# Kernel tuning notes

Hardware: AMD Instinct MI355X
Metric: run time of the kernel (lower is better)

The kernel has to match this reference:

```python
import jax, jax.numpy as jnp
import numpy as np
from jax import lax

T, B, H = 8192, 16, 256
D0, D1, D2 = 64, 64, 128


def setup_inputs() -> dict:
    key = jax.random.key(0)
    ks = jax.random.split(key, 16)
    k = 1.0 / np.sqrt(H)  # torch LSTMCell default init scale

    def u(kk, shape):
        return jax.random.uniform(kk, shape, jnp.float32, -k, k)

    inp = {
        "x0": jax.random.normal(ks[0], (T, B, D0), jnp.float32),
        "x1": jax.random.normal(ks[1], (T // 2, B, D1), jnp.float32),
        "x2": jax.random.normal(ks[2], (T // 4, B, D2), jnp.float32),
    }
    # one LSTMCell per possible concatenated input size: a=256 (all), b=128 (two), c=64 (one)
    sizes = [("a", D0 + D1 + D2), ("b", D0 + D1), ("c", D0)]
    i = 3
    for name, s in sizes:
        inp[f"W_ih_{name}"] = u(ks[i], (4 * H, s)); i += 1
        inp[f"W_hh_{name}"] = u(ks[i], (4 * H, H)); i += 1
        inp[f"b_ih_{name}"] = u(ks[i], (4 * H,)); i += 1
        inp[f"b_hh_{name}"] = u(ks[i], (4 * H,)); i += 1
    return inp


def _cell(x, h, c, Wih, Whh, bih, bhh):
    # torch.nn.LSTMCell: gates = x W_ih^T + b_ih + h W_hh^T + b_hh; order i,f,g,o
    g = x @ Wih.T + bih + h @ Whh.T + bhh
    i, f, gg, o = jnp.split(g, 4, axis=-1)
    c2 = jax.nn.sigmoid(f) * c + jax.nn.sigmoid(i) * jnp.tanh(gg)
    h2 = jax.nn.sigmoid(o) * jnp.tanh(c2)
    return h2, c2


def reference(x0, x1, x2,
              W_ih_a, W_hh_a, b_ih_a, b_hh_a,
              W_ih_b, W_hh_b, b_ih_b, b_hh_b,
              W_ih_c, W_hh_c, b_ih_c, b_hh_c):
    # ratios = [1, 2, 4]; active sets are nested: t%4==0 -> all 3, t%2==0 -> first 2, else first only
    def step(carry, t):
        h, c = carry

        def br_all(_):
            xt = jnp.concatenate([x0[t], x1[t // 2], x2[t // 4]], axis=-1)  # [B, 256]
            return _cell(xt, h, c, W_ih_a, W_hh_a, b_ih_a, b_hh_a)

        def br_two(_):
            xt = jnp.concatenate([x0[t], x1[t // 2]], axis=-1)  # [B, 128]
            return _cell(xt, h, c, W_ih_b, W_hh_b, b_ih_b, b_hh_b)

        def br_one(_):
            return _cell(x0[t], h, c, W_ih_c, W_hh_c, b_ih_c, b_hh_c)  # [B, 64]

        branch = jnp.where(t % 4 == 0, 0, jnp.where(t % 2 == 0, 1, 2))
        h2, c2 = lax.switch(branch, [br_all, br_two, br_one], None)
        return (h2, c2), h2

    h0 = jnp.zeros((B, H), jnp.float32)
    (_, _), ys = lax.scan(step, (h0, h0), jnp.arange(T))
    return ys  # [T, B, H]
```

## Files before the change

kernel.cpp:

```cpp
#include <hip/hip_runtime.h>
#include <stdint.h>


typedef _Float16 half8 __attribute__((ext_vector_type(8)));
typedef float floatx4 __attribute__((ext_vector_type(4)));
typedef unsigned int u32x4 __attribute__((ext_vector_type(4)));

#define T_STEPS 8192
#define NWG 16

__device__ __forceinline__ float fsig(float x) {
    return __builtin_amdgcn_rcpf(1.0f + __expf(-x));
}
__device__ __forceinline__ float ftanh(float x) {
    return 1.0f - 2.0f * __builtin_amdgcn_rcpf(1.0f + __expf(2.0f * x));
}

__device__ __forceinline__ half8 cvt8(floatx4 a, floatx4 b) {
    half8 h;
    h[0] = (_Float16)a[0]; h[1] = (_Float16)a[1]; h[2] = (_Float16)a[2]; h[3] = (_Float16)a[3];
    h[4] = (_Float16)b[0]; h[5] = (_Float16)b[1]; h[6] = (_Float16)b[2]; h[7] = (_Float16)b[3];
    return h;
}
__device__ __forceinline__ half8 ld8w(const float* p) {
    floatx4 a = *(const floatx4*)p;
    floatx4 b = *(const floatx4*)(p + 4);
    return cvt8(a, b);
}

__device__ __forceinline__ void ld64_sc1(const void* p, u32x4& a, u32x4& b, u32x4& c, u32x4& d) {
    asm volatile(
        "global_load_dwordx4 %0, %4, off sc1\n\t"
        "global_load_dwordx4 %1, %4, off offset:16 sc1\n\t"
        "global_load_dwordx4 %2, %4, off offset:32 sc1\n\t"
        "global_load_dwordx4 %3, %4, off offset:48 sc1\n\t"
        "s_waitcnt vmcnt(0)"
        : "=&v"(a), "=&v"(b), "=&v"(c), "=&v"(d)
        : "v"(p)
        : "memory");
}
__device__ __forceinline__ void st16_sc1(void* p, u32x4 v) {
    asm volatile("global_store_dwordx4 %0, %1, off sc1" :: "v"(p), "v"(v) : "memory");
}

__global__ __launch_bounds__(256, 1) void lstm_kernel(
    const float* __restrict__ x0, const float* __restrict__ x1, const float* __restrict__ x2,
    const float* __restrict__ Wih_a, const float* __restrict__ Whh_a,
    const float* __restrict__ bih_a, const float* __restrict__ bhh_a,
    const float* __restrict__ Wih_b, const float* __restrict__ Whh_b,
    const float* __restrict__ bih_b, const float* __restrict__ bhh_b,
    const float* __restrict__ Wih_c, const float* __restrict__ Whh_c,
    const float* __restrict__ bih_c, const float* __restrict__ bhh_c,
    float* __restrict__ out, uint8_t* __restrict__ ws, int smask)
{
    const int tid = threadIdx.x;
    const int g   = blockIdx.x;
    const int w   = tid >> 6;
    const int l   = tid & 63;
    const int n   = l & 15;
    const int mg  = l >> 4;
    const int up  = n & 3;
    const int gt  = n >> 2;
    const int unit = g * 16 + w * 4 + up;
    const int R    = gt * 256 + unit;

    uint8_t* hring = ws;

    __shared__ _Float16 XB[2][16][264];
    __shared__ _Float16 HB[16][264];

    half8 wfa[16], wfb[12], wfc[10];
    {
        const int ko = mg * 8;
        #pragma unroll
        for (int kt = 0; kt < 8; ++kt) wfa[kt]     = ld8w(Wih_a + (size_t)R * 256 + kt * 32 + ko);
        #pragma unroll
        for (int kt = 0; kt < 8; ++kt) wfa[8 + kt] = ld8w(Whh_a + (size_t)R * 256 + kt * 32 + ko);
        #pragma unroll
        for (int kt = 0; kt < 4; ++kt) wfb[kt]     = ld8w(Wih_b + (size_t)R * 128 + kt * 32 + ko);
        #pragma unroll
        for (int kt = 0; kt < 8; ++kt) wfb[4 + kt] = ld8w(Whh_b + (size_t)R * 256 + kt * 32 + ko);
        #pragma unroll
        for (int kt = 0; kt < 2; ++kt) wfc[kt]     = ld8w(Wih_c + (size_t)R * 64  + kt * 32 + ko);
        #pragma unroll
        for (int kt = 0; kt < 8; ++kt) wfc[2 + kt] = ld8w(Whh_c + (size_t)R * 256 + kt * 32 + ko);
    }
    const float ba = bih_a[R] + bhh_a[R];
    const float bb = bih_b[R] + bhh_b[R];
    const float bc = bih_c[R] + bhh_c[R];

    const int pm  = (tid & 127) >> 3;
    const int pcg = (tid & 7) * 8;
    const int qm  = tid >> 4;
    const int qcg = (tid & 15) * 8;

    floatx4 z4 = {0.f, 0.f, 0.f, 0.f};
    floatx4 a0A = z4, a1A = z4, b0A = z4, b1A = z4;
    floatx4 a0B = z4, a1B = z4, b0B = z4, b1B = z4;

    auto issue = [&](int ts, floatx4& A0, floatx4& A1, floatx4& B0, floatx4& B1) {
        const int brn = ((ts & 3) == 0) ? 0 : (((ts & 1) == 0) ? 1 : 2);
        if (tid < 128) {
            const floatx4* s = (const floatx4*)(x0 + (size_t)ts * 1024 + pm * 64 + pcg);
            A0 = s[0]; A1 = s[1];
        } else if (brn < 2) {
            const floatx4* s = (const floatx4*)(x1 + (size_t)(ts >> 1) * 1024 + pm * 64 + pcg);
            A0 = s[0]; A1 = s[1];
        }
        if (brn == 0) {
            const floatx4* s = (const floatx4*)(x2 + (size_t)(ts >> 2) * 2048 + qm * 128 + qcg);
            B0 = s[0]; B1 = s[1];
        }
    };
    auto stage = [&](int ts, floatx4 A0, floatx4 A1, floatx4 B0, floatx4 B1) {
        const int brn = ((ts & 3) == 0) ? 0 : (((ts & 1) == 0) ? 1 : 2);
        const int xb  = ts & 1;
        if (tid < 128)     *(half8*)&XB[xb][pm][pcg]       = cvt8(A0, A1);
        else if (brn < 2)  *(half8*)&XB[xb][pm][64 + pcg]  = cvt8(A0, A1);
        if (brn == 0)      *(half8*)&XB[xb][qm][128 + qcg] = cvt8(B0, B1);
    };

    {
        floatx4 A0 = z4, A1 = z4, B0 = z4, B1 = z4;
        issue(0, A0, A1, B0, B1);
        stage(0, A0, A1, B0, B1);
    }
    issue(1, a0B, a1B, b0B, b1B);

    float cst[4] = {0.f, 0.f, 0.f, 0.f};

    for (int t = 0; t < T_STEPS; ++t) {
        __syncthreads();

        const int br = ((t & 3) == 0) ? 0 : (((t & 1) == 0) ? 1 : 2);
        const int ao = mg * 8;
        const int xb = t & 1;

        floatx4 ac0 = {0.f, 0.f, 0.f, 0.f}, ac1 = {0.f, 0.f, 0.f, 0.f};
        if (br == 0) {
            #pragma unroll
            for (int kt = 0; kt < 8; kt += 2) {
                ac0 = __builtin_amdgcn_mfma_f32_16x16x32_f16(
                    *(const half8*)&XB[xb][n][kt * 32 + ao], wfa[kt], ac0, 0, 0, 0);
                ac1 = __builtin_amdgcn_mfma_f32_16x16x32_f16(
                    *(const half8*)&XB[xb][n][(kt + 1) * 32 + ao], wfa[kt + 1], ac1, 0, 0, 0);
            }
        } else if (br == 1) {
            #pragma unroll
            for (int kt = 0; kt < 4; kt += 2) {
                ac0 = __builtin_amdgcn_mfma_f32_16x16x32_f16(
                    *(const half8*)&XB[xb][n][kt * 32 + ao], wfb[kt], ac0, 0, 0, 0);
                ac1 = __builtin_amdgcn_mfma_f32_16x16x32_f16(
                    *(const half8*)&XB[xb][n][(kt + 1) * 32 + ao], wfb[kt + 1], ac1, 0, 0, 0);
            }
        } else {
            ac0 = __builtin_amdgcn_mfma_f32_16x16x32_f16(
                *(const half8*)&XB[xb][n][ao], wfc[0], ac0, 0, 0, 0);
            ac1 = __builtin_amdgcn_mfma_f32_16x16x32_f16(
                *(const half8*)&XB[xb][n][32 + ao], wfc[1], ac1, 0, 0, 0);
        }

        {
            const int row = tid >> 4, u = tid & 15;
            _Float16* dst = &HB[row][u * 16];
            if (t == 0) {
                *(u32x4*)dst       = (u32x4)0u;
                *(u32x4*)(dst + 8) = (u32x4)0u;
            } else {
                const uint32_t want = (uint32_t)t;
                const uint8_t* src = hring + (size_t)((t - 1) & smask) * 16384
                                   + (size_t)row * 1024 + (size_t)u * 64;
                u32x4 a, b, c, d;
                for (;;) {
                    ld64_sc1(src, a, b, c, d);
                    if (a[1] == want && a[3] == want && b[1] == want && b[3] == want &&
                        c[1] == want && c[3] == want && d[1] == want && d[3] == want)
                        break;
                }
                u32x4 lo = {a[0], a[2], b[0], b[2]};
                u32x4 hi = {c[0], c[2], d[0], d[2]};
                *(u32x4*)dst       = lo;
                *(u32x4*)(dst + 8) = hi;
            }
        }

        if (t + 2 < T_STEPS) {
            if ((t & 1) == 0) issue(t + 2, a0A, a1A, b0A, b1A);
            else              issue(t + 2, a0B, a1B, b0B, b1B);
        }

        __syncthreads();

        if (br == 0) {
            #pragma unroll
            for (int kt = 0; kt < 8; kt += 2) {
                ac0 = __builtin_amdgcn_mfma_f32_16x16x32_f16(
                    *(const half8*)&HB[n][kt * 32 + ao], wfa[8 + kt], ac0, 0, 0, 0);
                ac1 = __builtin_amdgcn_mfma_f32_16x16x32_f16(
                    *(const half8*)&HB[n][(kt + 1) * 32 + ao], wfa[9 + kt], ac1, 0, 0, 0);
            }
        } else if (br == 1) {
            #pragma unroll
            for (int kt = 0; kt < 8; kt += 2) {
                ac0 = __builtin_amdgcn_mfma_f32_16x16x32_f16(
                    *(const half8*)&HB[n][kt * 32 + ao], wfb[4 + kt], ac0, 0, 0, 0);
                ac1 = __builtin_amdgcn_mfma_f32_16x16x32_f16(
                    *(const half8*)&HB[n][(kt + 1) * 32 + ao], wfb[5 + kt], ac1, 0, 0, 0);
            }
        } else {
            #pragma unroll
            for (int kt = 0; kt < 8; kt += 2) {
                ac0 = __builtin_amdgcn_mfma_f32_16x16x32_f16(
                    *(const half8*)&HB[n][kt * 32 + ao], wfc[2 + kt], ac0, 0, 0, 0);
                ac1 = __builtin_amdgcn_mfma_f32_16x16x32_f16(
                    *(const half8*)&HB[n][(kt + 1) * 32 + ao], wfc[3 + kt], ac1, 0, 0, 0);
            }
        }
        const floatx4 acc = ac0 + ac1;

        const float bsel = (br == 0) ? ba : ((br == 1) ? bb : bc);
        float tv[4];
        #pragma unroll
        for (int r = 0; r < 4; ++r) {
            const float gv = acc[r] + bsel;
            tv[r] = (gt == 2) ? ftanh(gv) : fsig(gv);
        }
        float h2v[4];
        const int b0 = l & ~12;
        #pragma unroll
        for (int r = 0; r < 4; ++r) {
            const float vi = __shfl(tv[r], b0,      64);
            const float vf = __shfl(tv[r], b0 + 4,  64);
            const float vg = __shfl(tv[r], b0 + 8,  64);
            const float vo = __shfl(tv[r], b0 + 12, 64);
            const float c2 = vf * cst[r] + vi * vg;
            cst[r] = c2;
            h2v[r] = vo * ftanh(c2);
        }

        {
            uint8_t* sb = hring + (size_t)(t & smask) * 16384 + (size_t)(8 * g + 2 * w) * 8;
            const int s0 = l & ~15;
            #pragma unroll
            for (int r = 0; r < 4; ++r) {
                const unsigned hv =
                    (unsigned)__builtin_bit_cast(unsigned short, (_Float16)h2v[r]);
                const unsigned v0 = (unsigned)__shfl((int)hv, s0,     64);
                const unsigned v1 = (unsigned)__shfl((int)hv, s0 + 1, 64);
                const unsigned v2 = (unsigned)__shfl((int)hv, s0 + 2, 64);
                const unsigned v3 = (unsigned)__shfl((int)hv, s0 + 3, 64);
                if (n == 0) {
                    u32x4 pk = { (v0 & 0xffffu) | (v1 << 16), (unsigned)(t + 1),
                                 (v2 & 0xffffu) | (v3 << 16), (unsigned)(t + 1) };
                    st16_sc1(sb + (size_t)(mg * 4 + r) * 1024, pk);
                }
            }
        }

        if (gt == 0) {
            float* op = out + (size_t)t * 4096 + (size_t)(mg * 4) * 256 + unit;
            #pragma unroll
            for (int r = 0; r < 4; ++r) op[r * 256] = h2v[r];
        }

        if (t + 1 < T_STEPS) {
            if (t & 1) stage(t + 1, a0A, a1A, b0A, b1A);
            else       stage(t + 1, a0B, a1B, b0B, b1B);
        }
    }
}

extern "C" void kernel_launch(void* const* d_in, const int* in_sizes, int n_in,
                              void* d_out, int out_size, void* d_ws, size_t ws_size,
                              hipStream_t stream) {
    (void)in_sizes; (void)n_in; (void)out_size;
    const int smask = (ws_size >= 4 * 16384) ? 3 : 1;
    hipLaunchKernelGGL(lstm_kernel, dim3(NWG), dim3(256), 0, stream,
        (const float*)d_in[0], (const float*)d_in[1], (const float*)d_in[2],
        (const float*)d_in[3], (const float*)d_in[4], (const float*)d_in[5], (const float*)d_in[6],
        (const float*)d_in[7], (const float*)d_in[8], (const float*)d_in[9], (const float*)d_in[10],
        (const float*)d_in[11], (const float*)d_in[12], (const float*)d_in[13], (const float*)d_in[14],
        (float*)d_out, (uint8_t*)d_ws, smask);
}
```

Before: 20.01 ms.

## Gather h publish through LDS into one wave and defer output stores

Each step's new h fragment is now written to a small LDS staging tile and published to the global ring by a single wave with one 16-byte store per lane, instead of shuffles plus scattered stores from every wave. Wave 3 no longer polls the ring. Waves 0-1 poll as before, and wave 2 polls a double-width region so rows 8-15 are still covered. The output store for step t is deferred to the next iteration, so it overlaps the poll instead of sitting on the critical path. Barriers become a raw s_barrier that waits only on LDS counters. The cost is an extra barrier per step and more load imbalance among the polling waves.

```diff
diff --git a/kernel.cpp b/kernel.cpp
--- a/kernel.cpp
+++ b/kernel.cpp
@@ -14,6 +14,12 @@
 }
 __device__ __forceinline__ float ftanh(float x) {
     return 1.0f - 2.0f * __builtin_amdgcn_rcpf(1.0f + __expf(2.0f * x));
+}
+
+__device__ __forceinline__ void bar_lds() {
+    asm volatile("s_waitcnt lgkmcnt(0)" ::: "memory");
+    __builtin_amdgcn_s_barrier();
+    asm volatile("" ::: "memory");
 }
 
 __device__ __forceinline__ half8 cvt8(floatx4 a, floatx4 b) {
@@ -36,6 +42,24 @@
         "global_load_dwordx4 %3, %4, off offset:48 sc1\n\t"
         "s_waitcnt vmcnt(0)"
         : "=&v"(a), "=&v"(b), "=&v"(c), "=&v"(d)
+        : "v"(p)
+        : "memory");
+}
+__device__ __forceinline__ void ld128_sc1(const void* p,
+        u32x4& r0, u32x4& r1, u32x4& r2, u32x4& r3,
+        u32x4& r4, u32x4& r5, u32x4& r6, u32x4& r7) {
+    asm volatile(
+        "global_load_dwordx4 %0, %8, off sc1\n\t"
+        "global_load_dwordx4 %1, %8, off offset:16 sc1\n\t"
+        "global_load_dwordx4 %2, %8, off offset:32 sc1\n\t"
+        "global_load_dwordx4 %3, %8, off offset:48 sc1\n\t"
+        "global_load_dwordx4 %4, %8, off offset:64 sc1\n\t"
+        "global_load_dwordx4 %5, %8, off offset:80 sc1\n\t"
+        "global_load_dwordx4 %6, %8, off offset:96 sc1\n\t"
+        "global_load_dwordx4 %7, %8, off offset:112 sc1\n\t"
+        "s_waitcnt vmcnt(0)"
+        : "=&v"(r0), "=&v"(r1), "=&v"(r2), "=&v"(r3),
+          "=&v"(r4), "=&v"(r5), "=&v"(r6), "=&v"(r7)
         : "v"(p)
         : "memory");
 }
@@ -68,6 +92,7 @@
 
     __shared__ _Float16 XB[2][16][264];
     __shared__ _Float16 HB[16][264];
+    __shared__ _Float16 PUB[16][16];
 
     half8 wfa[16], wfb[12], wfc[10];
     {
@@ -127,10 +152,11 @@
     }
     issue(1, a0B, a1B, b0B, b1B);
 
-    float cst[4] = {0.f, 0.f, 0.f, 0.f};
+    float cst[4]    = {0.f, 0.f, 0.f, 0.f};
+    float h2prev[4] = {0.f, 0.f, 0.f, 0.f};
 
     for (int t = 0; t < T_STEPS; ++t) {
-        __syncthreads();
+        bar_lds();
 
         const int br = ((t & 3) == 0) ? 0 : (((t & 1) == 0) ? 1 : 2);
         const int ao = mg * 8;
@@ -160,28 +186,66 @@
                 *(const half8*)&XB[xb][n][32 + ao], wfc[1], ac1, 0, 0, 0);
         }
 
-        {
-            const int row = tid >> 4, u = tid & 15;
-            _Float16* dst = &HB[row][u * 16];
-            if (t == 0) {
-                *(u32x4*)dst       = (u32x4)0u;
-                *(u32x4*)(dst + 8) = (u32x4)0u;
+        if (w < 3) {
+            if (w < 2) {
+                const int row = tid >> 4, u = tid & 15;
+                _Float16* dst = &HB[row][u * 16];
+                if (t == 0) {
+                    *(u32x4*)dst       = (u32x4)0u;
+                    *(u32x4*)(dst + 8) = (u32x4)0u;
+                } else {
+                    const uint32_t want = (uint32_t)t;
+                    const uint8_t* src = hring + (size_t)((t - 1) & smask) * 16384
+                                       + (size_t)row * 1024 + (size_t)u * 64;
+                    u32x4 a, b, c, d;
+                    for (;;) {
+                        ld64_sc1(src, a, b, c, d);
+                        if (a[1] == want && a[3] == want && b[1] == want && b[3] == want &&
+                            c[1] == want && c[3] == want && d[1] == want && d[3] == want)
+                            break;
+                    }
+                    u32x4 lo = {a[0], a[2], b[0], b[2]};
+                    u32x4 hi = {c[0], c[2], d[0], d[2]};
+                    *(u32x4*)dst       = lo;
+                    *(u32x4*)(dst + 8) = hi;
+                }
             } else {
-                const uint32_t want = (uint32_t)t;
-                const uint8_t* src = hring + (size_t)((t - 1) & smask) * 16384
-                                   + (size_t)row * 1024 + (size_t)u * 64;
-                u32x4 a, b, c, d;
-                for (;;) {
-                    ld64_sc1(src, a, b, c, d);
-                    if (a[1] == want && a[3] == want && b[1] == want && b[3] == want &&
-                        c[1] == want && c[3] == want && d[1] == want && d[3] == want)
-                        break;
+                const int row = 8 + (l >> 3), u = (l & 7) * 2;
+                _Float16* dst = &HB[row][u * 16];
+                if (t == 0) {
+                    *(u32x4*)dst        = (u32x4)0u;
+                    *(u32x4*)(dst + 8)  = (u32x4)0u;
+                    *(u32x4*)(dst + 16) = (u32x4)0u;
+                    *(u32x4*)(dst + 24) = (u32x4)0u;
+                } else {
+                    const uint32_t want = (uint32_t)t;
+                    const uint8_t* src = hring + (size_t)((t - 1) & smask) * 16384
+                                       + (size_t)row * 1024 + (size_t)u * 64;
+                    u32x4 r0, r1, r2, r3, r4, r5, r6, r7;
+                    for (;;) {
+                        ld128_sc1(src, r0, r1, r2, r3, r4, r5, r6, r7);
+                        if (r0[1] == want && r0[3] == want && r1[1] == want && r1[3] == want &&
+                            r2[1] == want && r2[3] == want && r3[1] == want && r3[3] == want &&
+                            r4[1] == want && r4[3] == want && r5[1] == want && r5[3] == want &&
+                            r6[1] == want && r6[3] == want && r7[1] == want && r7[3] == want)
+                            break;
+                    }
+                    u32x4 d0 = {r0[0], r0[2], r1[0], r1[2]};
+                    u32x4 d1 = {r2[0], r2[2], r3[0], r3[2]};
+                    u32x4 d2 = {r4[0], r4[2], r5[0], r5[2]};
+                    u32x4 d3 = {r6[0], r6[2], r7[0], r7[2]};
+                    *(u32x4*)dst        = d0;
+                    *(u32x4*)(dst + 8)  = d1;
+                    *(u32x4*)(dst + 16) = d2;
+                    *(u32x4*)(dst + 24) = d3;
                 }
-                u32x4 lo = {a[0], a[2], b[0], b[2]};
-                u32x4 hi = {c[0], c[2], d[0], d[2]};
-                *(u32x4*)dst       = lo;
-                *(u32x4*)(dst + 8) = hi;
-            }
+            }
+        }
+
+        if (t > 0 && gt == 0) {
+            float* op = out + (size_t)(t - 1) * 4096 + (size_t)(mg * 4) * 256 + unit;
+            #pragma unroll
+            for (int r = 0; r < 4; ++r) op[r * 256] = h2prev[r];
         }
 
         if (t + 2 < T_STEPS) {
@@ -189,7 +253,7 @@
             else              issue(t + 2, a0B, a1B, b0B, b1B);
         }
 
-        __syncthreads();
+        bar_lds();
 
         if (br == 0) {
             #pragma unroll
@@ -238,35 +302,36 @@
             h2v[r] = vo * ftanh(c2);
         }
 
-        {
-            uint8_t* sb = hring + (size_t)(t & smask) * 16384 + (size_t)(8 * g + 2 * w) * 8;
-            const int s0 = l & ~15;
-            #pragma unroll
-            for (int r = 0; r < 4; ++r) {
-                const unsigned hv =
-                    (unsigned)__builtin_bit_cast(unsigned short, (_Float16)h2v[r]);
-                const unsigned v0 = (unsigned)__shfl((int)hv, s0,     64);
-                const unsigned v1 = (unsigned)__shfl((int)hv, s0 + 1, 64);
-                const unsigned v2 = (unsigned)__shfl((int)hv, s0 + 2, 64);
-                const unsigned v3 = (unsigned)__shfl((int)hv, s0 + 3, 64);
-                if (n == 0) {
-                    u32x4 pk = { (v0 & 0xffffu) | (v1 << 16), (unsigned)(t + 1),
-                                 (v2 & 0xffffu) | (v3 << 16), (unsigned)(t + 1) };
-                    st16_sc1(sb + (size_t)(mg * 4 + r) * 1024, pk);
-                }
-            }
-        }
-
-        if (gt == 0) {
-            float* op = out + (size_t)t * 4096 + (size_t)(mg * 4) * 256 + unit;
-            #pragma unroll
-            for (int r = 0; r < 4; ++r) op[r * 256] = h2v[r];
+        if (n < 4) {
+            #pragma unroll
+            for (int r = 0; r < 4; ++r)
+                PUB[mg * 4 + r][w * 4 + n] = (_Float16)h2v[r];
+        }
+        #pragma unroll
+        for (int r = 0; r < 4; ++r) h2prev[r] = h2v[r];
+
+        bar_lds();
+
+        if (w == 3) {
+            const int row = l >> 2, cp = l & 3;
+            const unsigned d0 = *(const unsigned*)&PUB[row][cp * 4];
+            const unsigned d1 = *(const unsigned*)&PUB[row][cp * 4 + 2];
+            u32x4 pk = { d0, (unsigned)(t + 1), d1, (unsigned)(t + 1) };
+            uint8_t* sb = hring + (size_t)(t & smask) * 16384
+                        + (size_t)row * 1024 + (size_t)(8 * g + 2 * cp) * 8;
+            st16_sc1(sb, pk);
         }
 
         if (t + 1 < T_STEPS) {
             if (t & 1) stage(t + 1, a0A, a1A, b0A, b1A);
             else       stage(t + 1, a0B, a1B, b0B, b1B);
         }
+    }
+
+    if (gt == 0) {
+        float* op = out + (size_t)(T_STEPS - 1) * 4096 + (size_t)(mg * 4) * 256 + unit;
+        #pragma unroll
+        for (int r = 0; r < 4; ++r) op[r * 256] = h2prev[r];
     }
 }
 
```

After: 21.03 ms. 1.05x slower.
